# Performance work log

Measured on AMD Instinct MI355X. Metric: run time of the kernel, lower is better.

## Reference

```python
import jax, jax.numpy as jnp
import numpy as np
from jax import lax

NPOINT = 1024
RADIUS = 0.4
NSAMPLE = 32


def _fps(xyz, m):
    """Farthest point sampling. xyz: (B,N,3) -> idx (B,m) int32."""
    B, N, _ = xyz.shape
    init_idx = jnp.zeros((B,), jnp.int32)

    def step(carry, _):
        dists, last = carry  # dists (B,N), last (B,)
        last_pt = jnp.take_along_axis(xyz, last[:, None, None], axis=1)  # (B,1,3)
        d = jnp.sum((xyz - last_pt) ** 2, axis=-1)  # (B,N)
        dists = jnp.minimum(dists, d)
        nxt = jnp.argmax(dists, axis=-1).astype(jnp.int32)
        return (dists, nxt), nxt

    (_, _), rest = lax.scan(step, (jnp.full((B, N), 1e10, jnp.float32), init_idx),
                            None, length=m - 1)
    return jnp.concatenate([init_idx[None, :], rest], axis=0).T  # (B,m)


def _ball_query(xyz, new_xyz, radius, k):
    """First-k in-radius neighbors (CUDA ball_query semantics: pad with first hit).
    xyz (B,N,3), new_xyz (B,M,3) -> (B,M,k) int32."""
    N = xyz.shape[1]
    d2 = jnp.sum((new_xyz[:, :, None, :] - xyz[:, None, :, :]) ** 2, axis=-1)  # (B,M,N)
    idx = jnp.where(d2 < radius * radius, jnp.arange(N, dtype=jnp.int32), jnp.int32(N))
    neg_topk, _ = lax.top_k(-idx, k)        # k smallest indices
    idx_k = -neg_topk                        # (B,M,k), invalid == N
    valid = idx_k < N
    first = idx_k[..., :1]                   # first (closest-index) hit
    return jnp.where(valid, idx_k, first)


def _gather(pts, idx):
    """pts (B,N,D), idx (B,M,K) -> (B,M,K,D)."""
    return jax.vmap(lambda p, i: p[i])(pts, idx)


def setup_inputs() -> dict:
    key = jax.random.key(0)
    ks = jax.random.split(key, 6)
    B, N, C = 8, 8192, 64
    cin = C + 3
    xyz = jax.random.normal(ks[0], (B, N, 3), jnp.float32)
    features = jax.random.normal(ks[1], (B, N, C), jnp.float32)
    w1 = jax.random.normal(ks[2], (64, cin), jnp.float32) * 0.05
    b1 = jnp.zeros((64,), jnp.float32)
    w2 = jax.random.normal(ks[3], (64, 64), jnp.float32) * 0.05
    b2 = jnp.zeros((64,), jnp.float32)
    w3 = jax.random.normal(ks[4], (128, 64), jnp.float32) * 0.05
    b3 = jnp.zeros((128,), jnp.float32)
    return {"xyz": xyz, "features": features, "w1": w1, "b1": b1,
            "w2": w2, "b2": b2, "w3": w3, "b3": b3}


def reference(xyz, features, w1, b1, w2, b2, w3, b3):
    # FPS sample npoint centers (pool=True branch)
    fps_idx = _fps(xyz, NPOINT)                                   # (B,M)
    new_xyz = jnp.take_along_axis(xyz, fps_idx[..., None], axis=1)  # (B,M,3)
    # ball-query grouping with use_xyz=True (relative coords prepended)
    gidx = _ball_query(xyz, new_xyz, RADIUS, NSAMPLE)             # (B,M,K)
    gxyz = _gather(xyz, gidx) - new_xyz[:, :, None, :]            # (B,M,K,3)
    gfeat = _gather(features, gidx)                               # (B,M,K,C)
    x = jnp.concatenate([gxyz, gfeat], axis=-1)                   # (B,M,K,3+C)
    # shared MLP (1x1 convs) + ReLU
    h = jax.nn.relu(jnp.einsum('bmkc,oc->bmko', x, w1) + b1)
    h = jax.nn.relu(jnp.einsum('bmkc,oc->bmko', h, w2) + b2)
    h = jax.nn.relu(jnp.einsum('bmkc,oc->bmko', h, w3) + b3)      # (B,M,K,128)
    # max-pool over group dim -> (B, C_out, M) like torch (B, mlp[-1], npoint)
    new_features = jnp.transpose(jnp.max(h, axis=2), (0, 2, 1))
    return new_xyz, new_features
```

## Files before the change

### kernel.cpp

```cpp
#include <hip/hip_runtime.h>
#include <stdint.h>

#define BB 8
#define NN 8192
#define NPOINT 1024
#define NSAMPLE 32
#define XS 104
#define HS 72

typedef short short8 __attribute__((ext_vector_type(8)));
typedef float floatx4 __attribute__((ext_vector_type(4)));

__device__ __forceinline__ unsigned short f2bf(float f) {
    unsigned u = __float_as_uint(f);
    unsigned r = u + 0x7FFFu + ((u >> 16) & 1u);
    return (unsigned short)(r >> 16);
}

__device__ __forceinline__ unsigned long long u64max(unsigned long long a,
                                                     unsigned long long b) {
    return (a > b) ? a : b;
}

template <int CTRL, int RMASK>
__device__ __forceinline__ unsigned long long dpp_max_step(unsigned long long key) {
    int lo = (int)(unsigned int)(key & 0xffffffffull);
    int hi = (int)(unsigned int)(key >> 32);
    int tlo = __builtin_amdgcn_update_dpp(0, lo, CTRL, RMASK, 0xF, true);
    int thi = __builtin_amdgcn_update_dpp(0, hi, CTRL, RMASK, 0xF, true);
    unsigned long long t = ((unsigned long long)(unsigned int)thi << 32) |
                           (unsigned long long)(unsigned int)tlo;
    return u64max(key, t);
}

__device__ __forceinline__ unsigned long long dpp_wave_max(unsigned long long key) {
    key = dpp_max_step<0x111, 0xF>(key);
    key = dpp_max_step<0x112, 0xF>(key);
    key = dpp_max_step<0x114, 0xF>(key);
    key = dpp_max_step<0x118, 0xF>(key);
    key = dpp_max_step<0x142, 0xA>(key);
    key = dpp_max_step<0x143, 0xC>(key);
    return key;
}

__global__ __launch_bounds__(512) void fps_kernel(const float* __restrict__ xyz,
                                                  float* __restrict__ new_xyz) {
    __shared__ float sx[NN];
    __shared__ float sy[NN];
    __shared__ float sz[NN];
    __shared__ __align__(16) unsigned long long wred[2][8];

    const int b = blockIdx.x;
    const int t = threadIdx.x;
    const int lane = t & 63;
    const int wv = t >> 6;
    const float* base = xyz + (size_t)b * NN * 3;

    float px[16], py[16], pz[16], dist[16];
#pragma unroll
    for (int i = 0; i < 16; ++i) {
        int p = t + (i << 9);
        float x = base[p * 3 + 0];
        float y = base[p * 3 + 1];
        float z = base[p * 3 + 2];
        sx[p] = x; sy[p] = y; sz[p] = z;
        px[i] = x; py[i] = y; pz[i] = z;
        dist[i] = 1e10f;
    }
    __syncthreads();

    float lx = sx[0], ly = sy[0], lz = sz[0];
    float* outb = new_xyz + (size_t)b * NPOINT * 3;
    if (t == 0) { outb[0] = lx; outb[1] = ly; outb[2] = lz; }

    for (int j = 1; j < NPOINT; ++j) {
        float bd = -1.0f;
        int bi = 0;
#pragma unroll
        for (int i = 0; i < 16; ++i) {
            float dx = __fsub_rn(px[i], lx);
            float dy = __fsub_rn(py[i], ly);
            float dz = __fsub_rn(pz[i], lz);
            float d2 = __fadd_rn(__fadd_rn(__fmul_rn(dx, dx), __fmul_rn(dy, dy)),
                                 __fmul_rn(dz, dz));
            float dd = fminf(dist[i], d2);
            dist[i] = dd;
            bool gt = dd > bd;
            bd = gt ? dd : bd;
            bi = gt ? i : bi;
        }
        int gi = t + (bi << 9);
        unsigned long long key =
            ((unsigned long long)__float_as_uint(bd) << 32) |
            (unsigned long long)(~(unsigned int)gi);
        key = dpp_wave_max(key);
        if (lane == 63) wred[j & 1][wv] = key;
        __syncthreads();
        int cur;
        {
            const unsigned long long* wr = wred[j & 1];
            ulonglong2 p01 = *(const ulonglong2*)&wr[0];
            ulonglong2 p23 = *(const ulonglong2*)&wr[2];
            ulonglong2 p45 = *(const ulonglong2*)&wr[4];
            ulonglong2 p67 = *(const ulonglong2*)&wr[6];
            unsigned long long m =
                u64max(u64max(u64max(p01.x, p01.y), u64max(p23.x, p23.y)),
                       u64max(u64max(p45.x, p45.y), u64max(p67.x, p67.y)));
            cur = (int)(~(unsigned int)(m & 0xffffffffull));
        }
        lx = sx[cur]; ly = sy[cur]; lz = sz[cur];
        if (t == 0) {
            outb[j * 3 + 0] = lx;
            outb[j * 3 + 1] = ly;
            outb[j * 3 + 2] = lz;
        }
    }
}

__global__ __launch_bounds__(256) void ballq_kernel(const float* __restrict__ xyz,
                                                    const float* __restrict__ new_xyz,
                                                    int* __restrict__ gidx) {
    __shared__ int s_hits[4][NSAMPLE];
    const int t = threadIdx.x;
    const int lane = t & 63;
    const int wv = t >> 6;
    const int g = blockIdx.x * 4 + wv;
    const int bi = g >> 10;
    const float R2 = (float)(0.4 * 0.4);

    const float cx = new_xyz[g * 3 + 0];
    const float cy = new_xyz[g * 3 + 1];
    const float cz = new_xyz[g * 3 + 2];
    const float* base = xyz + (size_t)bi * NN * 3;

    int have = 0;
    for (int chunk = 0; chunk < (NN / 64) && have < NSAMPLE; ++chunk) {
        int p = (chunk << 6) + lane;
        float dx = __fsub_rn(cx, base[p * 3 + 0]);
        float dy = __fsub_rn(cy, base[p * 3 + 1]);
        float dz = __fsub_rn(cz, base[p * 3 + 2]);
        float d2 = __fadd_rn(__fadd_rn(__fmul_rn(dx, dx), __fmul_rn(dy, dy)),
                             __fmul_rn(dz, dz));
        bool in = d2 < R2;
        unsigned long long m = __ballot(in);
        int pre = __popcll(m & ((1ull << lane) - 1ull));
        int slot = have + pre;
        if (in && slot < NSAMPLE) s_hits[wv][slot] = p;
        have += (int)__popcll(m);
    }
    __syncthreads();
    if (lane < NSAMPLE) {
        int first = s_hits[wv][0];
        int v = (lane < have) ? s_hits[wv][lane] : first;
        gidx[(size_t)g * NSAMPLE + lane] = v;
    }
}

__global__ __launch_bounds__(256) void mlp_mfma_kernel(
    const float* __restrict__ xyz, const float* __restrict__ features,
    const float* __restrict__ w1, const float* __restrict__ b1,
    const float* __restrict__ w2, const float* __restrict__ b2,
    const float* __restrict__ w3, const float* __restrict__ b3,
    const float* __restrict__ new_xyz, const int* __restrict__ gidx,
    float* __restrict__ out_feat) {
    __shared__ __align__(16) unsigned short s_x[128 * XS];
    __shared__ __align__(16) unsigned short s_h[128 * HS];
    __shared__ __align__(16) unsigned short s_w12[11264];
    __shared__ int s_gi[128];

    const int t = threadIdx.x;
    const int lane = t & 63;
    const int w = t >> 6;
    const int col = lane & 15;
    const int quad = lane >> 4;
    const int blk = blockIdx.x;
    const int bi = blk >> 8;

    if (t < 128) s_gi[t] = gidx[blk * 128 + t];
    __syncthreads();

    {
        int o = t >> 2, part = t & 3;
        const float* w1r = w1 + o * 67;
#pragma unroll
        for (int i = 0; i < 26; ++i) {
            int c = part * 26 + i;
            float v = 0.0f;
            if (c < 64) v = w1r[3 + c];
            else if (c < 67) v = w1r[c - 64];
            s_w12[o * XS + c] = f2bf(v);
        }
        const float* w2r = w2 + o * 64 + part * 16;
#pragma unroll
        for (int i = 0; i < 8; ++i) {
            unsigned pk = (unsigned)f2bf(w2r[2 * i]) |
                          ((unsigned)f2bf(w2r[2 * i + 1]) << 16);
            *(unsigned*)&s_w12[6656 + o * HS + part * 16 + 2 * i] = pk;
        }
    }
    {
        int k = t >> 1, half = t & 1;
        int row = s_gi[k];
        const float4* frow =
            (const float4*)(features + ((size_t)bi * NN + row) * 64) + half * 8;
        unsigned short* xr = &s_x[k * XS + half * 32];
#pragma unroll
        for (int i = 0; i < 8; ++i) {
            float4 v = frow[i];
            unsigned lo = (unsigned)f2bf(v.x) | ((unsigned)f2bf(v.y) << 16);
            unsigned hi = (unsigned)f2bf(v.z) | ((unsigned)f2bf(v.w) << 16);
            *(uint2*)(xr + i * 4) = make_uint2(lo, hi);
        }
    }
    if (t < 128) {
        int k = t;
        int row = s_gi[k];
        int gg = (blk << 2) + (k >> 5);
        const float* pr = xyz + ((size_t)bi * NN + row) * 3;
        const float* cr = new_xyz + (size_t)gg * 3;
        s_x[k * XS + 64] = f2bf(pr[0] - cr[0]);
        s_x[k * XS + 65] = f2bf(pr[1] - cr[1]);
        s_x[k * XS + 66] = f2bf(pr[2] - cr[2]);
        s_x[k * XS + 67] = 0;
        unsigned* z = (unsigned*)&s_x[k * XS + 68];
#pragma unroll
        for (int i = 0; i < 14; ++i) z[i] = 0;
    }
    __syncthreads();

    const int mbase = w * 32;

    floatx4 acc[2][4] = {};
    for (int kk = 0; kk < 3; ++kk) {
        short8 a0 = *(const short8*)&s_x[(mbase + col) * XS + kk * 32 + quad * 8];
        short8 a1 = *(const short8*)&s_x[(mbase + 16 + col) * XS + kk * 32 + quad * 8];
#pragma unroll
        for (int nt = 0; nt < 4; ++nt) {
            short8 b = *(const short8*)&s_w12[(nt * 16 + col) * XS + kk * 32 + quad * 8];
            acc[0][nt] = __builtin_amdgcn_mfma_f32_16x16x32_bf16(a0, b, acc[0][nt], 0, 0, 0);
            acc[1][nt] = __builtin_amdgcn_mfma_f32_16x16x32_bf16(a1, b, acc[1][nt], 0, 0, 0);
        }
    }
#pragma unroll
    for (int nt = 0; nt < 4; ++nt) {
        float bb = b1[nt * 16 + col];
#pragma unroll
        for (int mt = 0; mt < 2; ++mt)
#pragma unroll
            for (int r = 0; r < 4; ++r) {
                float v = fmaxf(acc[mt][nt][r] + bb, 0.0f);
                s_h[(mbase + mt * 16 + quad * 4 + r) * HS + nt * 16 + col] = f2bf(v);
            }
    }
    __syncthreads();

    floatx4 acc2[2][4] = {};
    for (int kk = 0; kk < 2; ++kk) {
        short8 a0 = *(const short8*)&s_h[(mbase + col) * HS + kk * 32 + quad * 8];
        short8 a1 = *(const short8*)&s_h[(mbase + 16 + col) * HS + kk * 32 + quad * 8];
#pragma unroll
        for (int nt = 0; nt < 4; ++nt) {
            short8 b = *(const short8*)&s_w12[6656 + (nt * 16 + col) * HS + kk * 32 + quad * 8];
            acc2[0][nt] = __builtin_amdgcn_mfma_f32_16x16x32_bf16(a0, b, acc2[0][nt], 0, 0, 0);
            acc2[1][nt] = __builtin_amdgcn_mfma_f32_16x16x32_bf16(a1, b, acc2[1][nt], 0, 0, 0);
        }
    }
    unsigned short* s_h2 = s_x;
#pragma unroll
    for (int nt = 0; nt < 4; ++nt) {
        float bb = b2[nt * 16 + col];
#pragma unroll
        for (int mt = 0; mt < 2; ++mt)
#pragma unroll
            for (int r = 0; r < 4; ++r) {
                float v = fmaxf(acc2[mt][nt][r] + bb, 0.0f);
                s_h2[(mbase + mt * 16 + quad * 4 + r) * HS + nt * 16 + col] = f2bf(v);
            }
    }
    __syncthreads();

    {
        int o = t >> 1, half = t & 1;
        const float* w3r = w3 + o * 64 + half * 32;
#pragma unroll
        for (int i = 0; i < 16; ++i) {
            unsigned pk = (unsigned)f2bf(w3r[2 * i]) |
                          ((unsigned)f2bf(w3r[2 * i + 1]) << 16);
            *(unsigned*)&s_w12[o * HS + half * 32 + 2 * i] = pk;
        }
    }
    __syncthreads();

    floatx4 c3[2][8] = {};
    for (int kk = 0; kk < 2; ++kk) {
        short8 a0 = *(const short8*)&s_h2[(mbase + col) * HS + kk * 32 + quad * 8];
        short8 a1 = *(const short8*)&s_h2[(mbase + 16 + col) * HS + kk * 32 + quad * 8];
#pragma unroll
        for (int nt = 0; nt < 8; ++nt) {
            short8 b = *(const short8*)&s_w12[(nt * 16 + col) * HS + kk * 32 + quad * 8];
            c3[0][nt] = __builtin_amdgcn_mfma_f32_16x16x32_bf16(a0, b, c3[0][nt], 0, 0, 0);
            c3[1][nt] = __builtin_amdgcn_mfma_f32_16x16x32_bf16(a1, b, c3[1][nt], 0, 0, 0);
        }
    }
    {
        int gg = (blk << 2) + w;
        float* ob = out_feat + (size_t)bi * (128 * 1024) + (gg & 1023);
#pragma unroll
        for (int nt = 0; nt < 8; ++nt) {
            float m = fmaxf(fmaxf(fmaxf(c3[0][nt][0], c3[0][nt][1]),
                                  fmaxf(c3[0][nt][2], c3[0][nt][3])),
                            fmaxf(fmaxf(c3[1][nt][0], c3[1][nt][1]),
                                  fmaxf(c3[1][nt][2], c3[1][nt][3])));
            m = fmaxf(m, __shfl_xor(m, 16));
            m = fmaxf(m, __shfl_xor(m, 32));
            if (lane < 16) {
                float v = fmaxf(m + b3[nt * 16 + lane], 0.0f);
                ob[(size_t)(nt * 16 + lane) * 1024] = v;
            }
        }
    }
}

extern "C" void kernel_launch(void* const* d_in, const int* in_sizes, int n_in,
                              void* d_out, int out_size, void* d_ws, size_t ws_size,
                              hipStream_t stream) {
    const float* xyz      = (const float*)d_in[0];
    const float* features = (const float*)d_in[1];
    const float* w1       = (const float*)d_in[2];
    const float* b1       = (const float*)d_in[3];
    const float* w2       = (const float*)d_in[4];
    const float* b2       = (const float*)d_in[5];
    const float* w3       = (const float*)d_in[6];
    const float* b3       = (const float*)d_in[7];

    float* out      = (float*)d_out;
    float* new_xyz  = out;
    float* out_feat = out + BB * NPOINT * 3;
    int*   gidx     = (int*)d_ws;

    fps_kernel<<<BB, 512, 0, stream>>>(xyz, new_xyz);
    ballq_kernel<<<(BB * NPOINT) / 4, 256, 0, stream>>>(xyz, new_xyz, gidx);
    mlp_mfma_kernel<<<(BB * NPOINT) / 4, 256, 0, stream>>>(xyz, features, w1, b1,
                                                           w2, b2, w3, b3,
                                                           new_xyz, gidx, out_feat);
}
```

Before: 1.113 ms.

## Fuse ball query into MLP kernel and halve FPS block size

Ball query now runs inside the MLP kernel: each wave writes its neighbour indices straight into shared memory, so the separate launch and the global gidx round trip go away. Separately, FPS now uses 256 threads with 32 points per thread and two independent argmax chains. With 4 waves instead of 8, the per-iteration barrier and cross-wave reduction should be cheaper, at the cost of more serial work per thread and higher register pressure.

```diff
diff --git a/kernel.cpp b/kernel.cpp
--- a/kernel.cpp
+++ b/kernel.cpp
@@ -43,12 +43,12 @@
     return key;
 }
 
-__global__ __launch_bounds__(512) void fps_kernel(const float* __restrict__ xyz,
-                                                  float* __restrict__ new_xyz) {
+__global__ __launch_bounds__(256, 1) void fps_kernel(const float* __restrict__ xyz,
+                                                     float* __restrict__ new_xyz) {
     __shared__ float sx[NN];
     __shared__ float sy[NN];
     __shared__ float sz[NN];
-    __shared__ __align__(16) unsigned long long wred[2][8];
+    __shared__ __align__(16) unsigned long long wred[2][4];
 
     const int b = blockIdx.x;
     const int t = threadIdx.x;
@@ -56,10 +56,10 @@
     const int wv = t >> 6;
     const float* base = xyz + (size_t)b * NN * 3;
 
-    float px[16], py[16], pz[16], dist[16];
-#pragma unroll
-    for (int i = 0; i < 16; ++i) {
-        int p = t + (i << 9);
+    float px[32], py[32], pz[32], dist[32];
+#pragma unroll
+    for (int i = 0; i < 32; ++i) {
+        int p = t + (i << 8);
         float x = base[p * 3 + 0];
         float y = base[p * 3 + 1];
         float z = base[p * 3 + 2];
@@ -74,25 +74,42 @@
     if (t == 0) { outb[0] = lx; outb[1] = ly; outb[2] = lz; }
 
     for (int j = 1; j < NPOINT; ++j) {
-        float bd = -1.0f;
-        int bi = 0;
-#pragma unroll
-        for (int i = 0; i < 16; ++i) {
-            float dx = __fsub_rn(px[i], lx);
-            float dy = __fsub_rn(py[i], ly);
-            float dz = __fsub_rn(pz[i], lz);
-            float d2 = __fadd_rn(__fadd_rn(__fmul_rn(dx, dx), __fmul_rn(dy, dy)),
-                                 __fmul_rn(dz, dz));
-            float dd = fminf(dist[i], d2);
-            dist[i] = dd;
-            bool gt = dd > bd;
-            bd = gt ? dd : bd;
-            bi = gt ? i : bi;
-        }
-        int gi = t + (bi << 9);
-        unsigned long long key =
-            ((unsigned long long)__float_as_uint(bd) << 32) |
-            (unsigned long long)(~(unsigned int)gi);
+        float bd0 = -1.0f, bd1 = -1.0f;
+        int bi0 = 0, bi1 = 1;
+#pragma unroll
+        for (int i = 0; i < 32; i += 2) {
+            {
+                float dx = __fsub_rn(px[i], lx);
+                float dy = __fsub_rn(py[i], ly);
+                float dz = __fsub_rn(pz[i], lz);
+                float d2 = __fadd_rn(__fadd_rn(__fmul_rn(dx, dx), __fmul_rn(dy, dy)),
+                                     __fmul_rn(dz, dz));
+                float dd = fminf(dist[i], d2);
+                dist[i] = dd;
+                bool gt = dd > bd0;
+                bd0 = gt ? dd : bd0;
+                bi0 = gt ? i : bi0;
+            }
+            {
+                float dx = __fsub_rn(px[i + 1], lx);
+                float dy = __fsub_rn(py[i + 1], ly);
+                float dz = __fsub_rn(pz[i + 1], lz);
+                float d2 = __fadd_rn(__fadd_rn(__fmul_rn(dx, dx), __fmul_rn(dy, dy)),
+                                     __fmul_rn(dz, dz));
+                float dd = fminf(dist[i + 1], d2);
+                dist[i + 1] = dd;
+                bool gt = dd > bd1;
+                bd1 = gt ? dd : bd1;
+                bi1 = gt ? (i + 1) : bi1;
+            }
+        }
+        unsigned long long key0 =
+            ((unsigned long long)__float_as_uint(bd0) << 32) |
+            (unsigned long long)(~(unsigned int)(t + (bi0 << 8)));
+        unsigned long long key1 =
+            ((unsigned long long)__float_as_uint(bd1) << 32) |
+            (unsigned long long)(~(unsigned int)(t + (bi1 << 8)));
+        unsigned long long key = u64max(key0, key1);
         key = dpp_wave_max(key);
         if (lane == 63) wred[j & 1][wv] = key;
         __syncthreads();
@@ -101,11 +118,8 @@
             const unsigned long long* wr = wred[j & 1];
             ulonglong2 p01 = *(const ulonglong2*)&wr[0];
             ulonglong2 p23 = *(const ulonglong2*)&wr[2];
-            ulonglong2 p45 = *(const ulonglong2*)&wr[4];
-            ulonglong2 p67 = *(const ulonglong2*)&wr[6];
-            unsigned long long m =
-                u64max(u64max(u64max(p01.x, p01.y), u64max(p23.x, p23.y)),
-                       u64max(u64max(p45.x, p45.y), u64max(p67.x, p67.y)));
+            unsigned long long m = u64max(u64max(p01.x, p01.y),
+                                          u64max(p23.x, p23.y));
             cur = (int)(~(unsigned int)(m & 0xffffffffull));
         }
         lx = sx[cur]; ly = sy[cur]; lz = sz[cur];
@@ -117,52 +131,12 @@
     }
 }
 
-__global__ __launch_bounds__(256) void ballq_kernel(const float* __restrict__ xyz,
-                                                    const float* __restrict__ new_xyz,
-                                                    int* __restrict__ gidx) {
-    __shared__ int s_hits[4][NSAMPLE];
-    const int t = threadIdx.x;
-    const int lane = t & 63;
-    const int wv = t >> 6;
-    const int g = blockIdx.x * 4 + wv;
-    const int bi = g >> 10;
-    const float R2 = (float)(0.4 * 0.4);
-
-    const float cx = new_xyz[g * 3 + 0];
-    const float cy = new_xyz[g * 3 + 1];
-    const float cz = new_xyz[g * 3 + 2];
-    const float* base = xyz + (size_t)bi * NN * 3;
-
-    int have = 0;
-    for (int chunk = 0; chunk < (NN / 64) && have < NSAMPLE; ++chunk) {
-        int p = (chunk << 6) + lane;
-        float dx = __fsub_rn(cx, base[p * 3 + 0]);
-        float dy = __fsub_rn(cy, base[p * 3 + 1]);
-        float dz = __fsub_rn(cz, base[p * 3 + 2]);
-        float d2 = __fadd_rn(__fadd_rn(__fmul_rn(dx, dx), __fmul_rn(dy, dy)),
-                             __fmul_rn(dz, dz));
-        bool in = d2 < R2;
-        unsigned long long m = __ballot(in);
-        int pre = __popcll(m & ((1ull << lane) - 1ull));
-        int slot = have + pre;
-        if (in && slot < NSAMPLE) s_hits[wv][slot] = p;
-        have += (int)__popcll(m);
-    }
-    __syncthreads();
-    if (lane < NSAMPLE) {
-        int first = s_hits[wv][0];
-        int v = (lane < have) ? s_hits[wv][lane] : first;
-        gidx[(size_t)g * NSAMPLE + lane] = v;
-    }
-}
-
-__global__ __launch_bounds__(256) void mlp_mfma_kernel(
+__global__ __launch_bounds__(256) void fused_bq_mlp_kernel(
     const float* __restrict__ xyz, const float* __restrict__ features,
     const float* __restrict__ w1, const float* __restrict__ b1,
     const float* __restrict__ w2, const float* __restrict__ b2,
     const float* __restrict__ w3, const float* __restrict__ b3,
-    const float* __restrict__ new_xyz, const int* __restrict__ gidx,
-    float* __restrict__ out_feat) {
+    const float* __restrict__ new_xyz, float* __restrict__ out_feat) {
     __shared__ __align__(16) unsigned short s_x[128 * XS];
     __shared__ __align__(16) unsigned short s_h[128 * HS];
     __shared__ __align__(16) unsigned short s_w12[11264];
@@ -176,9 +150,6 @@
     const int blk = blockIdx.x;
     const int bi = blk >> 8;
 
-    if (t < 128) s_gi[t] = gidx[blk * 128 + t];
-    __syncthreads();
-
     {
         int o = t >> 2, part = t & 3;
         const float* w1r = w1 + o * 67;
@@ -198,6 +169,38 @@
             *(unsigned*)&s_w12[6656 + o * HS + part * 16 + 2 * i] = pk;
         }
     }
+
+    {
+        const int g = (blk << 2) + w;
+        const float R2 = (float)(0.4 * 0.4);
+        const float cx = new_xyz[g * 3 + 0];
+        const float cy = new_xyz[g * 3 + 1];
+        const float cz = new_xyz[g * 3 + 2];
+        const float* base = xyz + (size_t)bi * NN * 3;
+
+        int have = 0;
+        for (int chunk = 0; chunk < (NN / 64) && have < NSAMPLE; ++chunk) {
+            int p = (chunk << 6) + lane;
+            float dx = __fsub_rn(cx, base[p * 3 + 0]);
+            float dy = __fsub_rn(cy, base[p * 3 + 1]);
+            float dz = __fsub_rn(cz, base[p * 3 + 2]);
+            float d2 = __fadd_rn(__fadd_rn(__fmul_rn(dx, dx), __fmul_rn(dy, dy)),
+                                 __fmul_rn(dz, dz));
+            bool in = d2 < R2;
+            unsigned long long m = __ballot(in);
+            int pre = __popcll(m & ((1ull << lane) - 1ull));
+            int slot = have + pre;
+            if (in && slot < NSAMPLE) s_gi[w * NSAMPLE + slot] = p;
+            have += (int)__popcll(m);
+        }
+        if (lane < NSAMPLE) {
+            int first = s_gi[w * NSAMPLE];
+            int v = (lane < have) ? s_gi[w * NSAMPLE + lane] : first;
+            s_gi[w * NSAMPLE + lane] = v;
+        }
+    }
+    __syncthreads();
+
     {
         int k = t >> 1, half = t & 1;
         int row = s_gi[k];
@@ -336,11 +339,8 @@
     float* out      = (float*)d_out;
     float* new_xyz  = out;
     float* out_feat = out + BB * NPOINT * 3;
-    int*   gidx     = (int*)d_ws;
-
-    fps_kernel<<<BB, 512, 0, stream>>>(xyz, new_xyz);
-    ballq_kernel<<<(BB * NPOINT) / 4, 256, 0, stream>>>(xyz, new_xyz, gidx);
-    mlp_mfma_kernel<<<(BB * NPOINT) / 4, 256, 0, stream>>>(xyz, features, w1, b1,
-                                                           w2, b2, w3, b3,
-                                                           new_xyz, gidx, out_feat);
-}
+
+    fps_kernel<<<BB, 256, 0, stream>>>(xyz, new_xyz);
+    fused_bq_mlp_kernel<<<(BB * NPOINT) / 4, 256, 0, stream>>>(
+        xyz, features, w1, b1, w2, b2, w3, b3, new_xyz, out_feat);
+}
```

After: 1.192 ms. +7.1%, slower.
